# Kernel optimization log

Hardware: AMD Instinct MI355X
Metric: run time of the kernel (lower is better)

Reference implementation:

```python
import jax, jax.numpy as jnp
import numpy as np


def setup_inputs() -> dict:
    key = jax.random.key(0)
    k0, k1, k2, k3, k4 = jax.random.split(key, 5)
    B, L, P, K = 8, 512, 80000, 16  # batch, seq len, n pairs, n spline knots
    CA = jax.random.normal(k0, (B, L, 3), jnp.float32) * 5.0
    CB = CA + jax.random.normal(k1, (B, L, 3), jnp.float32)
    # spline coefficients per residue pair: [L, L, K-1 intervals, 4 poly coeffs]
    coeff = jax.random.normal(k2, (L, L, K - 1, 4), jnp.float32) * 0.1
    step = 15.0 * np.pi / 180.0
    cutoffs = jnp.asarray(np.linspace(-1.5 * step, np.pi + 1.5 * step, K), jnp.float32)
    x_idx = jax.random.randint(k3, (P,), 0, L, dtype=jnp.int32)
    y_idx = jax.random.randint(k4, (P,), 0, L, dtype=jnp.int32)
    return {"CA": CA, "CB": CB, "coeff": coeff, "cutoffs": cutoffs,
            "x_idx": x_idx, "y_idx": y_idx}


def reference(CA, CB, coeff, cutoffs, x_idx, y_idx):
    eps = 1e-6
    B = CA.shape[0]
    # gather pairwise coordinates: [B, P, 3] -> [B*P, 3]
    x_CA = CA[:, x_idx].reshape(-1, 3)
    x_CB = CB[:, x_idx].reshape(-1, 3)
    y_CB = CB[:, y_idx].reshape(-1, 3)
    # angle at x_CB between (x_CA - x_CB) and (y_CB - x_CB)
    x = x_CA - x_CB
    y = y_CB - x_CB
    nx = jnp.linalg.norm(x, axis=-1)
    ny = jnp.linalg.norm(y, axis=-1)
    valid = (nx > eps) & (ny > eps)
    denom = jnp.where(valid, nx * ny, 1.0)
    c = jnp.sum(x * y, axis=-1) / denom
    good = (1.0 - c * c) > eps
    m = valid & good  # torch filters; we mask contributions instead (sum-reduce is equivalent)
    c_safe = jnp.where(m, jnp.clip(c, -1.0 + 1e-7, 1.0 - 1e-7), 0.0)
    phi = jnp.arccos(c_safe)  # [B*P]
    # gather spline coefficients for each pair: [B*P, K-1, 4]
    xi = jnp.tile(x_idx, B)
    yi = jnp.tile(y_idx, B)
    cf = coeff[xi, yi]
    n_int = cf.shape[1]
    idx = jnp.clip(jnp.searchsorted(cutoffs, phi) - 1, 0, n_int - 1)  # interval index
    dx = phi - cutoffs[idx]
    csel = jnp.take_along_axis(cf, idx[:, None, None], axis=1)[:, 0, :]  # [B*P, 4]
    # cubic poly: c3 + c2*x + c1*x^2 + c0*x^3 (Horner)
    val = csel[:, 3] + dx * (csel[:, 2] + dx * (csel[:, 1] + dx * csel[:, 0]))
    return jnp.sum(jnp.where(m, val, 0.0))
```

## Files before the change

kernel.cpp:

```cpp
#include <hip/hip_runtime.h>


namespace {
constexpr int BATCH = 8;
constexpr int SEQL  = 512;
constexpr int NPAIR = 80000;
constexpr int NKNOT = 16;
constexpr int NINT  = 15;
constexpr int BLOCK = 256;
constexpr int TOTAL = BATCH * NPAIR;
constexpr int NBLK  = TOTAL / BLOCK;
}

__device__ inline float block_reduce_sum(float v) {
    __shared__ float lds[BLOCK / 64];
    #pragma unroll
    for (int o = 32; o > 0; o >>= 1) v += __shfl_down(v, o, 64);
    const int wave = threadIdx.x >> 6;
    const int lane = threadIdx.x & 63;
    if (lane == 0) lds[wave] = v;
    __syncthreads();
    if (wave == 0) {
        v = (lane < BLOCK / 64) ? lds[lane] : 0.0f;
        #pragma unroll
        for (int o = BLOCK / 128; o > 0; o >>= 1) v += __shfl_down(v, o, 64);
    }
    return v;
}

__global__ __launch_bounds__(BLOCK) void phi_main_kernel(
    const float* __restrict__ CA, const float* __restrict__ CB,
    const float* __restrict__ coeff, const float* __restrict__ cutoffs,
    const int* __restrict__ x_idx, const int* __restrict__ y_idx,
    float* __restrict__ partial)
{
    const int tid = blockIdx.x * BLOCK + threadIdx.x;
    const int p = tid >> 3;
    const int b = tid & 7;

    const int xi = x_idx[p];
    const int yi = y_idx[p];

    const float* pxa = CA + (size_t)(b * SEQL + xi) * 3;
    const float* pxb = CB + (size_t)(b * SEQL + xi) * 3;
    const float* pyb = CB + (size_t)(b * SEQL + yi) * 3;

    const float xax = pxa[0], xay = pxa[1], xaz = pxa[2];
    const float xbx = pxb[0], xby = pxb[1], xbz = pxb[2];
    const float ybx = pyb[0], yby = pyb[1], ybz = pyb[2];

    const float xx = xax - xbx, xy = xay - xby, xz = xaz - xbz;
    const float yx = ybx - xbx, yy = yby - xby, yz = ybz - xbz;

    const float nx = sqrtf(xx * xx + xy * xy + xz * xz);
    const float ny = sqrtf(yx * yx + yy * yy + yz * yz);

    const float eps = 1e-6f;
    const bool valid = (nx > eps) && (ny > eps);
    const float denom = valid ? nx * ny : 1.0f;
    const float c = (xx * yx + xy * yy + xz * yz) / denom;
    const bool good = (1.0f - c * c) > eps;
    const bool m = valid && good;

    float acc = 0.0f;
    if (m) {
        const float clip_hi = 1.0f - 1e-7f;
        const float cl = fminf(fmaxf(c, -clip_hi), clip_hi);
        const float phi = acosf(cl);

        int cnt = 0;
        float low = cutoffs[0];
        #pragma unroll
        for (int k = 0; k < NKNOT; ++k) {
            const float ck = cutoffs[k];
            const bool lt = ck < phi;
            cnt += lt ? 1 : 0;
            low = lt ? ck : low;
        }
        int idx = cnt - 1;
        idx = idx < 0 ? 0 : (idx > NINT - 1 ? NINT - 1 : idx);

        const float dx = phi - low;

        const float4 cf = *reinterpret_cast<const float4*>(
            coeff + ((size_t)(xi * SEQL + yi) * NINT + idx) * 4);

        acc = cf.w + dx * (cf.z + dx * (cf.y + dx * cf.x));
    }

    const float bsum = block_reduce_sum(acc);
    if (threadIdx.x == 0) partial[blockIdx.x] = bsum;
}

__global__ __launch_bounds__(BLOCK) void phi_reduce_kernel(
    const float* __restrict__ partial, float* __restrict__ out)
{
    float v = 0.0f;
    for (int i = threadIdx.x; i < NBLK; i += BLOCK) v += partial[i];
    const float total = block_reduce_sum(v);
    if (threadIdx.x == 0) out[0] = total;
}

extern "C" void kernel_launch(void* const* d_in, const int* in_sizes, int n_in,
                              void* d_out, int out_size, void* d_ws, size_t ws_size,
                              hipStream_t stream) {
    const float* CA      = (const float*)d_in[0];
    const float* CB      = (const float*)d_in[1];
    const float* coeff   = (const float*)d_in[2];
    const float* cutoffs = (const float*)d_in[3];
    const int*   x_idx   = (const int*)d_in[4];
    const int*   y_idx   = (const int*)d_in[5];
    float* out = (float*)d_out;
    float* partial = (float*)d_ws;

    phi_main_kernel<<<NBLK, BLOCK, 0, stream>>>(CA, CB, coeff, cutoffs,
                                                x_idx, y_idx, partial);
    phi_reduce_kernel<<<1, BLOCK, 0, stream>>>(partial, out);
}
```

Before: 108.1 us.

## Stage coordinates in LDS and use persistent grid with per-thread multi-item loop

Each block copies all CA/CB coordinates into shared memory in a residue-major, batch-interleaved layout, precomputing CA-CB, so the per-pair gathers hit LDS instead of global memory. The launch switches to a fixed grid of 256 blocks of 1024 threads, with each thread handling up to three items, and the final reduce shrinks to one pass over 256 partials. In exchange, every block reloads the full 96 KB of coordinates, and the large LDS footprint (about 96 KB per block) limits occupancy.

```diff
diff --git a/kernel.cpp b/kernel.cpp
--- a/kernel.cpp
+++ b/kernel.cpp
@@ -7,21 +7,24 @@
 constexpr int NPAIR = 80000;
 constexpr int NKNOT = 16;
 constexpr int NINT  = 15;
-constexpr int BLOCK = 256;
+constexpr int BLOCK = 1024;
+constexpr int GRID  = 256;
 constexpr int TOTAL = BATCH * NPAIR;
-constexpr int NBLK  = TOTAL / BLOCK;
+constexpr int STRIDE = BLOCK * GRID;
+constexpr int NITEM = 3;
+constexpr int NCOORD = SEQL * BATCH * 3;
 }
 
 __device__ inline float block_reduce_sum(float v) {
-    __shared__ float lds[BLOCK / 64];
+    __shared__ float red[BLOCK / 64];
     #pragma unroll
     for (int o = 32; o > 0; o >>= 1) v += __shfl_down(v, o, 64);
     const int wave = threadIdx.x >> 6;
     const int lane = threadIdx.x & 63;
-    if (lane == 0) lds[wave] = v;
+    if (lane == 0) red[wave] = v;
     __syncthreads();
     if (wave == 0) {
-        v = (lane < BLOCK / 64) ? lds[lane] : 0.0f;
+        v = (lane < BLOCK / 64) ? red[lane] : 0.0f;
         #pragma unroll
         for (int o = BLOCK / 128; o > 0; o >>= 1) v += __shfl_down(v, o, 64);
     }
@@ -34,71 +37,96 @@
     const int* __restrict__ x_idx, const int* __restrict__ y_idx,
     float* __restrict__ partial)
 {
-    const int tid = blockIdx.x * BLOCK + threadIdx.x;
-    const int p = tid >> 3;
-    const int b = tid & 7;
+    __shared__ float u_lds [NCOORD];
+    __shared__ float cb_lds[NCOORD];
 
-    const int xi = x_idx[p];
-    const int yi = y_idx[p];
-
-    const float* pxa = CA + (size_t)(b * SEQL + xi) * 3;
-    const float* pxb = CB + (size_t)(b * SEQL + xi) * 3;
-    const float* pyb = CB + (size_t)(b * SEQL + yi) * 3;
-
-    const float xax = pxa[0], xay = pxa[1], xaz = pxa[2];
-    const float xbx = pxb[0], xby = pxb[1], xbz = pxb[2];
-    const float ybx = pyb[0], yby = pyb[1], ybz = pyb[2];
-
-    const float xx = xax - xbx, xy = xay - xby, xz = xaz - xbz;
-    const float yx = ybx - xbx, yy = yby - xby, yz = ybz - xbz;
-
-    const float nx = sqrtf(xx * xx + xy * xy + xz * xz);
-    const float ny = sqrtf(yx * yx + yy * yy + yz * yz);
+    for (int i = threadIdx.x; i < NCOORD; i += BLOCK) {
+        const float ca = CA[i];
+        const float cb = CB[i];
+        const int b    = i / (SEQL * 3);
+        const int rem  = i - b * (SEQL * 3);
+        const int r    = rem / 3;
+        const int comp = rem - r * 3;
+        const int j    = (r * BATCH + b) * 3 + comp;
+        u_lds[j]  = ca - cb;
+        cb_lds[j] = cb;
+    }
+    __syncthreads();
 
     const float eps = 1e-6f;
-    const bool valid = (nx > eps) && (ny > eps);
-    const float denom = valid ? nx * ny : 1.0f;
-    const float c = (xx * yx + xy * yy + xz * yz) / denom;
-    const bool good = (1.0f - c * c) > eps;
-    const bool m = valid && good;
+    float acc = 0.0f;
 
-    float acc = 0.0f;
-    if (m) {
-        const float clip_hi = 1.0f - 1e-7f;
-        const float cl = fminf(fmaxf(c, -clip_hi), clip_hi);
-        const float phi = acosf(cl);
+    #pragma unroll
+    for (int k = 0; k < NITEM; ++k) {
+        const int item = blockIdx.x * BLOCK + threadIdx.x + k * STRIDE;
+        if (item < TOTAL) {
+            const int p = item >> 3;
+            const int b = item & 7;
+            const int xi = x_idx[p];
+            const int yi = y_idx[p];
 
-        int cnt = 0;
-        float low = cutoffs[0];
-        #pragma unroll
-        for (int k = 0; k < NKNOT; ++k) {
-            const float ck = cutoffs[k];
-            const bool lt = ck < phi;
-            cnt += lt ? 1 : 0;
-            low = lt ? ck : low;
+            const float* pu  = &u_lds [(xi * BATCH + b) * 3];
+            const float* pxb = &cb_lds[(xi * BATCH + b) * 3];
+            const float* pyb = &cb_lds[(yi * BATCH + b) * 3];
+
+            const float xx = pu[0],  xy = pu[1],  xz = pu[2];
+            const float xbx = pxb[0], xby = pxb[1], xbz = pxb[2];
+            const float ybx = pyb[0], yby = pyb[1], ybz = pyb[2];
+
+            const float yx = ybx - xbx, yy = yby - xby, yz = ybz - xbz;
+
+            const float nx = sqrtf(xx * xx + xy * xy + xz * xz);
+            const float ny = sqrtf(yx * yx + yy * yy + yz * yz);
+
+            const bool valid = (nx > eps) && (ny > eps);
+            const float denom = valid ? nx * ny : 1.0f;
+            const float c = (xx * yx + xy * yy + xz * yz) / denom;
+            const bool good = (1.0f - c * c) > eps;
+            const bool m = valid && good;
+
+            if (m) {
+                const float clip_hi = 1.0f - 1e-7f;
+                const float cl = fminf(fmaxf(c, -clip_hi), clip_hi);
+                const float phi = acosf(cl);
+
+                int cnt = 0;
+                float low = cutoffs[0];
+                #pragma unroll
+                for (int t = 0; t < NKNOT; ++t) {
+                    const float ck = cutoffs[t];
+                    const bool lt = ck < phi;
+                    cnt += lt ? 1 : 0;
+                    low = lt ? ck : low;
+                }
+                int idx = cnt - 1;
+                idx = idx < 0 ? 0 : (idx > NINT - 1 ? NINT - 1 : idx);
+
+                const float dx = phi - low;
+
+                const float4 cf = *reinterpret_cast<const float4*>(
+                    coeff + ((size_t)(xi * SEQL + yi) * NINT + idx) * 4);
+
+                acc += cf.w + dx * (cf.z + dx * (cf.y + dx * cf.x));
+            }
         }
-        int idx = cnt - 1;
-        idx = idx < 0 ? 0 : (idx > NINT - 1 ? NINT - 1 : idx);
-
-        const float dx = phi - low;
-
-        const float4 cf = *reinterpret_cast<const float4*>(
-            coeff + ((size_t)(xi * SEQL + yi) * NINT + idx) * 4);
-
-        acc = cf.w + dx * (cf.z + dx * (cf.y + dx * cf.x));
     }
 
     const float bsum = block_reduce_sum(acc);
     if (threadIdx.x == 0) partial[blockIdx.x] = bsum;
 }
 
-__global__ __launch_bounds__(BLOCK) void phi_reduce_kernel(
+__global__ __launch_bounds__(256) void phi_reduce_kernel(
     const float* __restrict__ partial, float* __restrict__ out)
 {
-    float v = 0.0f;
-    for (int i = threadIdx.x; i < NBLK; i += BLOCK) v += partial[i];
-    const float total = block_reduce_sum(v);
-    if (threadIdx.x == 0) out[0] = total;
+    float v = (threadIdx.x < GRID) ? partial[threadIdx.x] : 0.0f;
+    #pragma unroll
+    for (int o = 32; o > 0; o >>= 1) v += __shfl_down(v, o, 64);
+    __shared__ float red[4];
+    const int wave = threadIdx.x >> 6;
+    const int lane = threadIdx.x & 63;
+    if (lane == 0) red[wave] = v;
+    __syncthreads();
+    if (threadIdx.x == 0) out[0] = red[0] + red[1] + red[2] + red[3];
 }
 
 extern "C" void kernel_launch(void* const* d_in, const int* in_sizes, int n_in,
@@ -113,7 +141,7 @@
     float* out = (float*)d_out;
     float* partial = (float*)d_ws;
 
-    phi_main_kernel<<<NBLK, BLOCK, 0, stream>>>(CA, CB, coeff, cutoffs,
+    phi_main_kernel<<<GRID, BLOCK, 0, stream>>>(CA, CB, coeff, cutoffs,
                                                 x_idx, y_idx, partial);
-    phi_reduce_kernel<<<1, BLOCK, 0, stream>>>(partial, out);
+    phi_reduce_kernel<<<1, 256, 0, stream>>>(partial, out);
 }
```

Result: no change. 107.0 us (-1.1%).
